# Performance work log

Measured on AMD Instinct MI355X. Metric: run time of the kernel, lower is better.

## Reference

```python
import jax, jax.numpy as jnp
import numpy as np

B, S, D, H = 4, 1024, 1024, 16
DEPTH = D // H


def setup_inputs() -> dict:
    key = jax.random.key(0)
    ks = jax.random.split(key, 13)
    inp = {
        'query': jax.random.normal(ks[0], (B, S, D), dtype=jnp.float32),
        'key': jax.random.normal(ks[1], (B, S, D), dtype=jnp.float32),
        'value': jax.random.normal(ks[2], (B, S, D), dtype=jnp.float32),
        'mask': jax.random.bernoulli(ks[3], 0.1, (B, S, S)),
    }
    scale = 1.0 / np.sqrt(D)
    inp['wq_w'] = jax.random.uniform(ks[4], (D, D), jnp.float32, -scale, scale)
    inp['wq_b'] = jax.random.uniform(ks[5], (D,), jnp.float32, -scale, scale)
    inp['wk_w'] = jax.random.uniform(ks[6], (D, D), jnp.float32, -scale, scale)
    inp['wk_b'] = jax.random.uniform(ks[7], (D,), jnp.float32, -scale, scale)
    inp['wv_w'] = jax.random.uniform(ks[8], (D, D), jnp.float32, -scale, scale)
    inp['wv_b'] = jax.random.uniform(ks[9], (D,), jnp.float32, -scale, scale)
    inp['fc_w'] = jax.random.uniform(ks[10], (D, D), jnp.float32, -scale, scale)
    inp['fc_b'] = jax.random.uniform(ks[11], (D,), jnp.float32, -scale, scale)
    return inp


def _split_heads(x):
    # [B,S,D] -> [B,H,S,depth]
    b, s, _ = x.shape
    return x.reshape(b, s, H, DEPTH).transpose(0, 2, 1, 3)


def reference(query, key, value, mask, wq_w, wq_b, wk_w, wk_b, wv_w, wv_b, fc_w, fc_b):
    q = _split_heads(query @ wq_w.T + wq_b)
    k = _split_heads(key @ wk_w.T + wk_b)
    v = _split_heads(value @ wv_w.T + wv_b)
    scores = jnp.einsum('bhqd,bhkd->bhqk', q, k) / jnp.sqrt(jnp.float32(DEPTH))
    scores = jnp.where(mask[:, None, :, :], jnp.float32(-1e9), scores)
    attn = jax.nn.softmax(scores, axis=-1)
    out = jnp.einsum('bhqk,bhkd->bhqd', attn, v)  # [B,H,S,depth]
    out = out.transpose(0, 2, 1, 3).reshape(query.shape[0], -1, D)
    return out @ fc_w.T + fc_b
```

## Files before the change

kernel.cpp:

```cpp
#include <hip/hip_runtime.h>
#include <hip/hip_bf16.h>


typedef __bf16 bf16x8 __attribute__((ext_vector_type(8)));
typedef __bf16 bf16x4 __attribute__((ext_vector_type(4)));
typedef float  f32x4  __attribute__((ext_vector_type(4)));

typedef const __attribute__((address_space(1))) void* gptr_t;
typedef __attribute__((address_space(3))) void* lptr_t;

#define MFMA16(a, b, c) __builtin_amdgcn_mfma_f32_16x16x32_bf16((a), (b), (c), 0, 0, 0)

__device__ __forceinline__ void gload_lds16(const void* g, void* l) {
  __builtin_amdgcn_global_load_lds((gptr_t)g, (lptr_t)l, 16, 0, 0);
}

__global__ void detect_mask(const unsigned char* m, int* flag) {
  __shared__ int s1[256], s23[256];
  int tid = threadIdx.x;
  int c1 = 0, c23 = 0;
  for (int i = tid; i < 4096; i += 256) {
    int r = i & 3;
    if (m[i]) { if (r == 1) c1++; else if (r >= 2) c23++; }
  }
  s1[tid] = c1; s23[tid] = c23;
  __syncthreads();
  for (int st = 128; st; st >>= 1) {
    if (tid < st) { s1[tid] += s1[tid + st]; s23[tid] += s23[tid + st]; }
    __syncthreads();
  }
  if (tid == 0) *flag = (s1[0] > 0) ? 1 : (s23[0] > 0 ? 2 : 0);
}

__global__ void pack_mask(const void* m, const int* flag, unsigned int* out) {
  size_t i = (size_t)blockIdx.x * 256 + threadIdx.x;
  int f = *flag;
  bool v;
  if (f == 1)      v = ((const unsigned char*)m)[i] != 0;
  else if (f == 2) v = ((const float*)m)[i] != 0.0f;
  else             v = ((const int*)m)[i] != 0;
  unsigned long long bal = __ballot(v);
  int lane = threadIdx.x & 63;
  if ((lane & 31) == 0) out[i >> 5] = (unsigned int)(bal >> (lane & 32));
}

__global__ void cvt3(const float* a, const float* b, const float* c,
                     __bf16* oa, __bf16* ob, __bf16* oc) {
  int bid = blockIdx.x;
  int which = bid >> 12, sub = bid & 4095;
  const float* in = which == 0 ? a : which == 1 ? b : c;
  __bf16* out = which == 0 ? oa : which == 1 ? ob : oc;
  size_t i = (size_t)sub * 256 + threadIdx.x;
  float4 v = ((const float4*)in)[i];
  bf16x4 o; o[0] = (__bf16)v.x; o[1] = (__bf16)v.y; o[2] = (__bf16)v.z; o[3] = (__bf16)v.w;
  ((bf16x4*)out)[i] = o;
}

__global__ void cvt4(const float* a, const float* b, const float* c, const float* d,
                     __bf16* oa, __bf16* ob, __bf16* oc, __bf16* od) {
  int bid = blockIdx.x;
  int which = bid >> 10, sub = bid & 1023;
  const float* in = which == 0 ? a : which == 1 ? b : which == 2 ? c : d;
  __bf16* out = which == 0 ? oa : which == 1 ? ob : which == 2 ? oc : od;
  size_t i = (size_t)sub * 256 + threadIdx.x;
  float4 v = ((const float4*)in)[i];
  bf16x4 o; o[0] = (__bf16)v.x; o[1] = (__bf16)v.y; o[2] = (__bf16)v.z; o[3] = (__bf16)v.w;
  ((bf16x4*)out)[i] = o;
}

__global__ __launch_bounds__(256, 2)
void gemm_qkv(const __bf16* qb, const __bf16* kb, const __bf16* vb,
              const __bf16* wq, const __bf16* wk, const __bf16* wv,
              const float* bq, const float* bk, const float* bv,
              __bf16* Qp, __bf16* Kp, __bf16* Vt) {
  __shared__ __bf16 As[128 * 64];
  __shared__ __bf16 Bs[128 * 64];
  const int bm = blockIdx.x;
  const int bnall = blockIdx.y;
  const int which = bnall >> 3;
  const int bn = bnall & 7;
  const __bf16* A = which == 0 ? qb : which == 1 ? kb : vb;
  const __bf16* W = which == 0 ? wq : which == 1 ? wk : wv;
  const float* bias = which == 0 ? bq : which == 1 ? bk : bv;

  const int tid = threadIdx.x, wave = tid >> 6, lane = tid & 63;
  const int wr = wave >> 1, wc = wave & 1;
  const int rl = lane >> 3, c8 = lane & 7;
  f32x4 acc[4][4] = {};

  for (int kt = 0; kt < 16; ++kt) {
    __syncthreads();
#pragma unroll
    for (int i = 0; i < 4; ++i) {
      int row = wave * 32 + i * 8 + rl;
      int sw = (c8 ^ (row & 7)) << 3;
      gload_lds16(A + (size_t)(bm * 128 + row) * 1024 + kt * 64 + sw, As + (wave * 32 + i * 8) * 64);
      gload_lds16(W + (size_t)(bn * 128 + row) * 1024 + kt * 64 + sw, Bs + (wave * 32 + i * 8) * 64);
    }
    __syncthreads();
#pragma unroll
    for (int k32 = 0; k32 < 2; ++k32) {
      bf16x8 af[4], bfr[4];
#pragma unroll
      for (int mi = 0; mi < 4; ++mi) {
        int row = wr * 64 + mi * 16 + (lane & 15);
        af[mi] = *(const bf16x8*)(As + row * 64 + (((k32 * 4 + (lane >> 4)) ^ (row & 7)) << 3));
      }
#pragma unroll
      for (int ni = 0; ni < 4; ++ni) {
        int row = wc * 64 + ni * 16 + (lane & 15);
        bfr[ni] = *(const bf16x8*)(Bs + row * 64 + (((k32 * 4 + (lane >> 4)) ^ (row & 7)) << 3));
      }
#pragma unroll
      for (int mi = 0; mi < 4; ++mi)
#pragma unroll
        for (int ni = 0; ni < 4; ++ni)
          acc[mi][ni] = MFMA16(af[mi], bfr[ni], acc[mi][ni]);
    }
  }
  const int r0 = (lane >> 4) * 4, cl = lane & 15;
  __bf16* Onat = which == 0 ? Qp : Kp;
#pragma unroll
  for (int ni = 0; ni < 4; ++ni) {
    int col = bn * 128 + wc * 64 + ni * 16 + cl;
    float bvv = bias[col];
#pragma unroll
    for (int mi = 0; mi < 4; ++mi) {
      int rowb = bm * 128 + wr * 64 + mi * 16 + r0;
      if (which < 2) {
#pragma unroll
        for (int r = 0; r < 4; ++r)
          Onat[(size_t)(rowb + r) * 1024 + col] = (__bf16)(acc[mi][ni][r] + bvv);
      } else {
        int bb = rowb >> 10, s0 = rowb & 1023, hh = col >> 6, d = col & 63;
        bf16x4 ov;
#pragma unroll
        for (int r = 0; r < 4; ++r) ov[r] = (__bf16)(acc[mi][ni][r] + bvv);
        *(bf16x4*)(Vt + (((size_t)(bb * 16 + hh) * 64 + d) << 10) + s0) = ov;
      }
    }
  }
}

__global__ __launch_bounds__(256, 2)
void gemm_fc(const __bf16* A, const __bf16* W, const float* bias, float* C) {
  __shared__ __bf16 As[128 * 64];
  __shared__ __bf16 Bs[128 * 64];
  const int bm = blockIdx.x, bn = blockIdx.y;
  const int tid = threadIdx.x, wave = tid >> 6, lane = tid & 63;
  const int wr = wave >> 1, wc = wave & 1;
  const int rl = lane >> 3, c8 = lane & 7;
  f32x4 acc[4][4] = {};

  for (int kt = 0; kt < 16; ++kt) {
    __syncthreads();
#pragma unroll
    for (int i = 0; i < 4; ++i) {
      int row = wave * 32 + i * 8 + rl;
      int sw = (c8 ^ (row & 7)) << 3;
      gload_lds16(A + (size_t)(bm * 128 + row) * 1024 + kt * 64 + sw, As + (wave * 32 + i * 8) * 64);
      gload_lds16(W + (size_t)(bn * 128 + row) * 1024 + kt * 64 + sw, Bs + (wave * 32 + i * 8) * 64);
    }
    __syncthreads();
#pragma unroll
    for (int k32 = 0; k32 < 2; ++k32) {
      bf16x8 af[4], bfr[4];
#pragma unroll
      for (int mi = 0; mi < 4; ++mi) {
        int row = wr * 64 + mi * 16 + (lane & 15);
        af[mi] = *(const bf16x8*)(As + row * 64 + (((k32 * 4 + (lane >> 4)) ^ (row & 7)) << 3));
      }
#pragma unroll
      for (int ni = 0; ni < 4; ++ni) {
        int row = wc * 64 + ni * 16 + (lane & 15);
        bfr[ni] = *(const bf16x8*)(Bs + row * 64 + (((k32 * 4 + (lane >> 4)) ^ (row & 7)) << 3));
      }
#pragma unroll
      for (int mi = 0; mi < 4; ++mi)
#pragma unroll
        for (int ni = 0; ni < 4; ++ni)
          acc[mi][ni] = MFMA16(af[mi], bfr[ni], acc[mi][ni]);
    }
  }
  const int r0 = (lane >> 4) * 4, cl = lane & 15;
#pragma unroll
  for (int ni = 0; ni < 4; ++ni) {
    int col = bn * 128 + wc * 64 + ni * 16 + cl;
    float bvv = bias[col];
#pragma unroll
    for (int mi = 0; mi < 4; ++mi) {
      int rowb = bm * 128 + wr * 64 + mi * 16 + r0;
#pragma unroll
      for (int r = 0; r < 4; ++r)
        C[(size_t)(rowb + r) * 1024 + col] = acc[mi][ni][r] + bvv;
    }
  }
}

__global__ __launch_bounds__(256, 2)
void attn(const __bf16* Qp, const __bf16* Kp, const __bf16* Vt,
          const unsigned int* mp, __bf16* O) {
  __shared__ __bf16 Qs[128 * 64];
  __shared__ __bf16 Ks[128 * 64];
  __shared__ __bf16 Vs[64 * 128];
  __shared__ __bf16 Ps[128 * 128];
  const int tid = threadIdx.x, wave = tid >> 6, lane = tid & 63;
  const int bx = blockIdx.x;
  const int qt = bx & 7, h = (bx >> 3) & 15, b = bx >> 7;
  const int rl = lane >> 3, c8 = lane & 7;

#pragma unroll
  for (int i = 0; i < 4; ++i) {
    int row = wave * 32 + i * 8 + rl;
    int sw = (c8 ^ (row & 7)) << 3;
    gload_lds16(Qp + (size_t)(b * 1024 + qt * 128 + row) * 1024 + h * 64 + sw,
                Qs + (wave * 32 + i * 8) * 64);
  }
  __syncthreads();
  bf16x8 qf[2][2];
#pragma unroll
  for (int mi = 0; mi < 2; ++mi)
#pragma unroll
    for (int k32 = 0; k32 < 2; ++k32) {
      int row = wave * 32 + mi * 16 + (lane & 15);
      qf[mi][k32] = *(const bf16x8*)(Qs + row * 64 + (((k32 * 4 + (lane >> 4)) ^ (row & 7)) << 3));
    }

  f32x4 oacc[2][4] = {};
  float dsum[2][4] = {};
  const unsigned int* mrow_base = mp + ((size_t)(b << 10) + qt * 128) * 32;

  for (int kt = 0; kt < 8; ++kt) {
    __syncthreads();
#pragma unroll
    for (int i = 0; i < 4; ++i) {
      int row = wave * 32 + i * 8 + rl;
      int sw = (c8 ^ (row & 7)) << 3;
      gload_lds16(Kp + (size_t)(b * 1024 + kt * 128 + row) * 1024 + h * 64 + sw,
                  Ks + (wave * 32 + i * 8) * 64);
    }
#pragma unroll
    for (int i = 0; i < 4; ++i) {
      int d0 = wave * 16 + i * 4;
      int d = d0 + (lane >> 4), c16 = lane & 15;
      gload_lds16(Vt + (((size_t)(b * 16 + h) * 64 + d) << 10) + kt * 128 + ((c16 ^ (d & 7)) << 3),
                  Vs + d0 * 128);
    }
    __syncthreads();

    uint4 mw[2][4];
#pragma unroll
    for (int mi = 0; mi < 2; ++mi)
#pragma unroll
      for (int r = 0; r < 4; ++r) {
        int rowl = wave * 32 + mi * 16 + (lane >> 4) * 4 + r;
        mw[mi][r] = *(const uint4*)(mrow_base + (size_t)rowl * 32 + kt * 4);
      }

#pragma unroll
    for (int ni = 0; ni < 8; ++ni) {
      f32x4 s0 = {}, s1 = {};
#pragma unroll
      for (int k32 = 0; k32 < 2; ++k32) {
        int row = ni * 16 + (lane & 15);
        bf16x8 kf = *(const bf16x8*)(Ks + row * 64 + (((k32 * 4 + (lane >> 4)) ^ (row & 7)) << 3));
        s0 = MFMA16(qf[0][k32], kf, s0);
        s1 = MFMA16(qf[1][k32], kf, s1);
      }
      int col = ni * 16 + (lane & 15);
      int bit = (ni & 1) * 16 + (lane & 15);
      int wsel = ni >> 1;
#pragma unroll
      for (int mi = 0; mi < 2; ++mi) {
        f32x4 sv = mi ? s1 : s0;
#pragma unroll
        for (int r = 0; r < 4; ++r) {
          unsigned int w = ((const unsigned int*)&mw[mi][r])[wsel];
          float p = ((w >> bit) & 1) ? 0.0f : __expf(sv[r] * 0.125f);
          __bf16 pb = (__bf16)p;
          dsum[mi][r] += (float)pb;
          int rowl = wave * 32 + mi * 16 + (lane >> 4) * 4 + r;
          *(__bf16*)((char*)Ps + rowl * 256 + ((col * 2) ^ ((rowl & 7) << 4))) = pb;
        }
      }
    }

#pragma unroll
    for (int ks = 0; ks < 4; ++ks) {
      bf16x8 pf0, pf1;
      {
        int row = wave * 32 + (lane & 15);
        pf0 = *(const bf16x8*)((const char*)Ps + row * 256 + (((ks * 4 + (lane >> 4)) * 16) ^ ((row & 7) << 4)));
        row = wave * 32 + 16 + (lane & 15);
        pf1 = *(const bf16x8*)((const char*)Ps + row * 256 + (((ks * 4 + (lane >> 4)) * 16) ^ ((row & 7) << 4)));
      }
#pragma unroll
      for (int nd = 0; nd < 4; ++nd) {
        int d = nd * 16 + (lane & 15);
        bf16x8 vf = *(const bf16x8*)((const char*)Vs + d * 256 + (((ks * 4 + (lane >> 4)) * 16) ^ ((d & 7) << 4)));
        oacc[0][nd] = MFMA16(pf0, vf, oacc[0][nd]);
        oacc[1][nd] = MFMA16(pf1, vf, oacc[1][nd]);
      }
    }
  }

#pragma unroll
  for (int mi = 0; mi < 2; ++mi)
#pragma unroll
    for (int r = 0; r < 4; ++r) {
      float v = dsum[mi][r];
      v += __shfl_xor(v, 1, 64);
      v += __shfl_xor(v, 2, 64);
      v += __shfl_xor(v, 4, 64);
      v += __shfl_xor(v, 8, 64);
      dsum[mi][r] = v;
    }

#pragma unroll
  for (int mi = 0; mi < 2; ++mi)
#pragma unroll
    for (int nd = 0; nd < 4; ++nd)
#pragma unroll
      for (int r = 0; r < 4; ++r) {
        int rowl = wave * 32 + mi * 16 + (lane >> 4) * 4 + r;
        int d = nd * 16 + (lane & 15);
        float v = oacc[mi][nd][r] / dsum[mi][r];
        O[(size_t)(b * 1024 + qt * 128 + rowl) * 1024 + h * 64 + d] = (__bf16)v;
      }
}

extern "C" void kernel_launch(void* const* d_in, const int* in_sizes, int n_in,
                              void* d_out, int out_size, void* d_ws, size_t ws_size,
                              hipStream_t stream) {
  const float* query = (const float*)d_in[0];
  const float* key   = (const float*)d_in[1];
  const float* value = (const float*)d_in[2];
  const void*  mask  = d_in[3];
  const float* wq_w  = (const float*)d_in[4];
  const float* wq_b  = (const float*)d_in[5];
  const float* wk_w  = (const float*)d_in[6];
  const float* wk_b  = (const float*)d_in[7];
  const float* wv_w  = (const float*)d_in[8];
  const float* wv_b  = (const float*)d_in[9];
  const float* fc_w  = (const float*)d_in[10];
  const float* fc_b  = (const float*)d_in[11];

  char* ws = (char*)d_ws;
  __bf16* qb  = (__bf16*)ws;
  __bf16* kb  = qb  + 4194304;
  __bf16* vb  = kb  + 4194304;
  __bf16* wqb = vb  + 4194304;
  __bf16* wkb = wqb + 1048576;
  __bf16* wvb = wkb + 1048576;
  __bf16* fcb = wvb + 1048576;
  __bf16* Qp  = fcb + 1048576;
  __bf16* Kp  = Qp  + 4194304;
  __bf16* Vt  = Kp  + 4194304;
  __bf16* Ob  = Vt  + 4194304;
  unsigned int* mpk = (unsigned int*)(Ob + 4194304);
  int* flag = (int*)(mpk + 131072);

  detect_mask<<<1, 256, 0, stream>>>((const unsigned char*)mask, flag);
  pack_mask<<<16384, 256, 0, stream>>>(mask, flag, mpk);
  cvt3<<<12288, 256, 0, stream>>>(query, key, value, qb, kb, vb);
  cvt4<<<4096, 256, 0, stream>>>(wq_w, wk_w, wv_w, fc_w, wqb, wkb, wvb, fcb);
  dim3 g1(32, 24);
  gemm_qkv<<<g1, 256, 0, stream>>>(qb, kb, vb, wqb, wkb, wvb, wq_b, wk_b, wv_b, Qp, Kp, Vt);
  attn<<<512, 256, 0, stream>>>(Qp, Kp, Vt, mpk, Ob);
  dim3 g2(32, 8);
  gemm_fc<<<g2, 256, 0, stream>>>(Ob, fcb, fc_b, (float*)d_out);
}
```

Before: 245.7 us.

## Rewrite attention as LDS-free 32x32 MFMA kernel with register P exchange

Replaces the LDS-staged attention kernel with one that uses 32x32x16 bf16 MFMAs. It computes S^T so that the P tile can be rebuilt as an MFMA A-operand with a cross-half lane shuffle, and reads K and V fragments directly from global memory, with no shared memory or barriers. The softmax uses exp2 with a folded scale, and the mask detector becomes a single vectorized ballot. This removes LDS traffic and sync stalls, but relies on L2/L1 for the repeated K/V reads across the four waves and drops the occupancy hint.

```diff
diff --git a/kernel.cpp b/kernel.cpp
--- a/kernel.cpp
+++ b/kernel.cpp
@@ -5,31 +5,43 @@
 typedef __bf16 bf16x8 __attribute__((ext_vector_type(8)));
 typedef __bf16 bf16x4 __attribute__((ext_vector_type(4)));
 typedef float  f32x4  __attribute__((ext_vector_type(4)));
+typedef float  f32x16 __attribute__((ext_vector_type(16)));
 
 typedef const __attribute__((address_space(1))) void* gptr_t;
 typedef __attribute__((address_space(3))) void* lptr_t;
 
 #define MFMA16(a, b, c) __builtin_amdgcn_mfma_f32_16x16x32_bf16((a), (b), (c), 0, 0, 0)
+#define MFMA32(a, b, c) __builtin_amdgcn_mfma_f32_32x32x16_bf16((a), (b), (c), 0, 0, 0)
 
 __device__ __forceinline__ void gload_lds16(const void* g, void* l) {
   __builtin_amdgcn_global_load_lds((gptr_t)g, (lptr_t)l, 16, 0, 0);
 }
 
+__device__ __forceinline__ unsigned pack2(float a, float b) {
+  union { __bf16 h[2]; unsigned u; } x;
+  x.h[0] = (__bf16)a; x.h[1] = (__bf16)b; return x.u;
+}
+
+__device__ __forceinline__ bf16x8 mkfrag(unsigned a, unsigned b, unsigned c, unsigned d) {
+  union { unsigned w[4]; bf16x8 v; } x;
+  x.w[0] = a; x.w[1] = b; x.w[2] = c; x.w[3] = d; return x.v;
+}
+
 __global__ void detect_mask(const unsigned char* m, int* flag) {
-  __shared__ int s1[256], s23[256];
+  __shared__ int s1[4], s23[4];
   int tid = threadIdx.x;
-  int c1 = 0, c23 = 0;
-  for (int i = tid; i < 4096; i += 256) {
-    int r = i & 3;
-    if (m[i]) { if (r == 1) c1++; else if (r >= 2) c23++; }
-  }
-  s1[tid] = c1; s23[tid] = c23;
+  uint4 v = ((const uint4*)m)[tid];
+  unsigned x0 = v.x, x1 = v.y, x2 = v.z, x3 = v.w;
+  unsigned c1  = (x0 & 0x0000ff00u) | (x1 & 0x0000ff00u) | (x2 & 0x0000ff00u) | (x3 & 0x0000ff00u);
+  unsigned c23 = (x0 & 0xffff0000u) | (x1 & 0xffff0000u) | (x2 & 0xffff0000u) | (x3 & 0xffff0000u);
+  unsigned long long b1 = __ballot(c1 != 0), b23 = __ballot(c23 != 0);
+  if ((tid & 63) == 0) { s1[tid >> 6] = (b1 != 0); s23[tid >> 6] = (b23 != 0); }
   __syncthreads();
-  for (int st = 128; st; st >>= 1) {
-    if (tid < st) { s1[tid] += s1[tid + st]; s23[tid] += s23[tid + st]; }
-    __syncthreads();
-  }
-  if (tid == 0) *flag = (s1[0] > 0) ? 1 : (s23[0] > 0 ? 2 : 0);
+  if (tid == 0) {
+    int a1 = s1[0] | s1[1] | s1[2] | s1[3];
+    int a23 = s23[0] | s23[1] | s23[2] | s23[3];
+    *flag = a1 ? 1 : (a23 ? 2 : 0);
+  }
 }
 
 __global__ void pack_mask(const void* m, const int* flag, unsigned int* out) {
@@ -197,136 +209,113 @@
   }
 }
 
-__global__ __launch_bounds__(256, 2)
-void attn(const __bf16* Qp, const __bf16* Kp, const __bf16* Vt,
-          const unsigned int* mp, __bf16* O) {
-  __shared__ __bf16 Qs[128 * 64];
-  __shared__ __bf16 Ks[128 * 64];
-  __shared__ __bf16 Vs[64 * 128];
-  __shared__ __bf16 Ps[128 * 128];
+__global__ __launch_bounds__(256)
+void attn32(const __bf16* __restrict__ Qp, const __bf16* __restrict__ Kp,
+            const __bf16* __restrict__ Vt, const unsigned long long* __restrict__ mp64,
+            __bf16* __restrict__ O) {
   const int tid = threadIdx.x, wave = tid >> 6, lane = tid & 63;
+  const int lo5 = lane & 31, hi = lane >> 5;
   const int bx = blockIdx.x;
   const int qt = bx & 7, h = (bx >> 3) & 15, b = bx >> 7;
-  const int rl = lane >> 3, c8 = lane & 7;
-
-#pragma unroll
-  for (int i = 0; i < 4; ++i) {
-    int row = wave * 32 + i * 8 + rl;
-    int sw = (c8 ^ (row & 7)) << 3;
-    gload_lds16(Qp + (size_t)(b * 1024 + qt * 128 + row) * 1024 + h * 64 + sw,
-                Qs + (wave * 32 + i * 8) * 64);
-  }
-  __syncthreads();
-  bf16x8 qf[2][2];
-#pragma unroll
-  for (int mi = 0; mi < 2; ++mi)
-#pragma unroll
-    for (int k32 = 0; k32 < 2; ++k32) {
-      int row = wave * 32 + mi * 16 + (lane & 15);
-      qf[mi][k32] = *(const bf16x8*)(Qs + row * 64 + (((k32 * 4 + (lane >> 4)) ^ (row & 7)) << 3));
-    }
-
-  f32x4 oacc[2][4] = {};
-  float dsum[2][4] = {};
-  const unsigned int* mrow_base = mp + ((size_t)(b << 10) + qt * 128) * 32;
-
-  for (int kt = 0; kt < 8; ++kt) {
-    __syncthreads();
-#pragma unroll
-    for (int i = 0; i < 4; ++i) {
-      int row = wave * 32 + i * 8 + rl;
-      int sw = (c8 ^ (row & 7)) << 3;
-      gload_lds16(Kp + (size_t)(b * 1024 + kt * 128 + row) * 1024 + h * 64 + sw,
-                  Ks + (wave * 32 + i * 8) * 64);
-    }
-#pragma unroll
-    for (int i = 0; i < 4; ++i) {
-      int d0 = wave * 16 + i * 4;
-      int d = d0 + (lane >> 4), c16 = lane & 15;
-      gload_lds16(Vt + (((size_t)(b * 16 + h) * 64 + d) << 10) + kt * 128 + ((c16 ^ (d & 7)) << 3),
-                  Vs + d0 * 128);
-    }
-    __syncthreads();
-
-    uint4 mw[2][4];
-#pragma unroll
-    for (int mi = 0; mi < 2; ++mi)
-#pragma unroll
-      for (int r = 0; r < 4; ++r) {
-        int rowl = wave * 32 + mi * 16 + (lane >> 4) * 4 + r;
-        mw[mi][r] = *(const uint4*)(mrow_base + (size_t)rowl * 32 + kt * 4);
-      }
-
-#pragma unroll
-    for (int ni = 0; ni < 8; ++ni) {
-      f32x4 s0 = {}, s1 = {};
-#pragma unroll
-      for (int k32 = 0; k32 < 2; ++k32) {
-        int row = ni * 16 + (lane & 15);
-        bf16x8 kf = *(const bf16x8*)(Ks + row * 64 + (((k32 * 4 + (lane >> 4)) ^ (row & 7)) << 3));
-        s0 = MFMA16(qf[0][k32], kf, s0);
-        s1 = MFMA16(qf[1][k32], kf, s1);
-      }
-      int col = ni * 16 + (lane & 15);
-      int bit = (ni & 1) * 16 + (lane & 15);
-      int wsel = ni >> 1;
-#pragma unroll
-      for (int mi = 0; mi < 2; ++mi) {
-        f32x4 sv = mi ? s1 : s0;
-#pragma unroll
-        for (int r = 0; r < 4; ++r) {
-          unsigned int w = ((const unsigned int*)&mw[mi][r])[wsel];
-          float p = ((w >> bit) & 1) ? 0.0f : __expf(sv[r] * 0.125f);
-          __bf16 pb = (__bf16)p;
-          dsum[mi][r] += (float)pb;
-          int rowl = wave * 32 + mi * 16 + (lane >> 4) * 4 + r;
-          *(__bf16*)((char*)Ps + rowl * 256 + ((col * 2) ^ ((rowl & 7) << 4))) = pb;
-        }
-      }
-    }
-
-#pragma unroll
-    for (int ks = 0; ks < 4; ++ks) {
-      bf16x8 pf0, pf1;
-      {
-        int row = wave * 32 + (lane & 15);
-        pf0 = *(const bf16x8*)((const char*)Ps + row * 256 + (((ks * 4 + (lane >> 4)) * 16) ^ ((row & 7) << 4)));
-        row = wave * 32 + 16 + (lane & 15);
-        pf1 = *(const bf16x8*)((const char*)Ps + row * 256 + (((ks * 4 + (lane >> 4)) * 16) ^ ((row & 7) << 4)));
-      }
-#pragma unroll
-      for (int nd = 0; nd < 4; ++nd) {
-        int d = nd * 16 + (lane & 15);
-        bf16x8 vf = *(const bf16x8*)((const char*)Vs + d * 256 + (((ks * 4 + (lane >> 4)) * 16) ^ ((d & 7) << 4)));
-        oacc[0][nd] = MFMA16(pf0, vf, oacc[0][nd]);
-        oacc[1][nd] = MFMA16(pf1, vf, oacc[1][nd]);
-      }
-    }
-  }
-
-#pragma unroll
-  for (int mi = 0; mi < 2; ++mi)
-#pragma unroll
-    for (int r = 0; r < 4; ++r) {
-      float v = dsum[mi][r];
-      v += __shfl_xor(v, 1, 64);
-      v += __shfl_xor(v, 2, 64);
-      v += __shfl_xor(v, 4, 64);
-      v += __shfl_xor(v, 8, 64);
-      dsum[mi][r] = v;
-    }
-
-#pragma unroll
-  for (int mi = 0; mi < 2; ++mi)
-#pragma unroll
-    for (int nd = 0; nd < 4; ++nd)
-#pragma unroll
-      for (int r = 0; r < 4; ++r) {
-        int rowl = wave * 32 + mi * 16 + (lane >> 4) * 4 + r;
-        int d = nd * 16 + (lane & 15);
-        float v = oacc[mi][nd][r] / dsum[mi][r];
-        O[(size_t)(b * 1024 + qt * 128 + rowl) * 1024 + h * 64 + d] = (__bf16)v;
-      }
+  const int qrow = qt * 128 + wave * 32 + lo5;
+  const float SC = 0.18033688011112042f;
+
+  bf16x8 qf[4];
+  const __bf16* qb = Qp + ((size_t)(b * 1024 + qrow)) * 1024 + h * 64 + hi * 8;
+#pragma unroll
+  for (int m = 0; m < 4; ++m) qf[m] = *(const bf16x8*)(qb + m * 16);
+
+  f32x16 oacc0 = {}, oacc1 = {};
+  float dsum = 0.0f;
+  const unsigned long long* mrow = mp64 + ((size_t)(b * 1024 + qrow)) * 16;
+  const __bf16* vrow = Vt + ((size_t)((b * 16 + h) * 64 + lo5)) * 1024;
+
+  for (int kt = 0; kt < 16; ++kt) {
+    unsigned long long mw = mrow[kt];
+    const __bf16* kb = Kp + ((size_t)(b * 1024 + kt * 64 + lo5)) * 1024 + h * 64 + hi * 8;
+    const __bf16* vb = vrow + kt * 64 + hi * 8;
+
+    f32x16 s0 = {};
+#pragma unroll
+    for (int m = 0; m < 4; ++m)
+      s0 = MFMA32(*(const bf16x8*)(kb + m * 16), qf[m], s0);
+    float p0[16];
+#pragma unroll
+    for (int r = 0; r < 16; ++r) {
+      int cr = (r & 3) + 8 * (r >> 2) + 4 * hi;
+      float e = exp2f(s0[r] * SC);
+      p0[r] = ((mw >> cr) & 1) ? 0.0f : e;
+      dsum += p0[r];
+    }
+    unsigned own0[8], rcv0[8];
+#pragma unroll
+    for (int u = 0; u < 4; ++u) {
+      own0[2 * u]     = pack2(p0[4 * u],     p0[4 * u + 1]);
+      own0[2 * u + 1] = pack2(p0[4 * u + 2], p0[4 * u + 3]);
+    }
+#pragma unroll
+    for (int i = 0; i < 8; ++i) rcv0[i] = (unsigned)__shfl_xor((int)own0[i], 32, 64);
+#pragma unroll
+    for (int s = 0; s < 2; ++s) {
+      const int ue2 = 4 * s, uo2 = 4 * s + 2;
+      unsigned fw0 = hi ? rcv0[uo2 + 0] : own0[ue2 + 0];
+      unsigned fw1 = hi ? rcv0[uo2 + 1] : own0[ue2 + 1];
+      unsigned fw2 = hi ? own0[uo2 + 0] : rcv0[ue2 + 0];
+      unsigned fw3 = hi ? own0[uo2 + 1] : rcv0[ue2 + 1];
+      bf16x8 pa = mkfrag(fw0, fw1, fw2, fw3);
+      bf16x8 vf0 = *(const bf16x8*)(vb + s * 16);
+      bf16x8 vf1 = *(const bf16x8*)(vb + s * 16 + 32 * 1024);
+      oacc0 = MFMA32(pa, vf0, oacc0);
+      oacc1 = MFMA32(pa, vf1, oacc1);
+    }
+
+    f32x16 s1 = {};
+#pragma unroll
+    for (int m = 0; m < 4; ++m)
+      s1 = MFMA32(*(const bf16x8*)(kb + 32 * 1024 + m * 16), qf[m], s1);
+    float p1[16];
+#pragma unroll
+    for (int r = 0; r < 16; ++r) {
+      int cr = (r & 3) + 8 * (r >> 2) + 4 * hi;
+      float e = exp2f(s1[r] * SC);
+      p1[r] = ((mw >> (32 + cr)) & 1) ? 0.0f : e;
+      dsum += p1[r];
+    }
+    unsigned own1[8], rcv1[8];
+#pragma unroll
+    for (int u = 0; u < 4; ++u) {
+      own1[2 * u]     = pack2(p1[4 * u],     p1[4 * u + 1]);
+      own1[2 * u + 1] = pack2(p1[4 * u + 2], p1[4 * u + 3]);
+    }
+#pragma unroll
+    for (int i = 0; i < 8; ++i) rcv1[i] = (unsigned)__shfl_xor((int)own1[i], 32, 64);
+#pragma unroll
+    for (int s = 0; s < 2; ++s) {
+      const int ue2 = 4 * s, uo2 = 4 * s + 2;
+      unsigned fw0 = hi ? rcv1[uo2 + 0] : own1[ue2 + 0];
+      unsigned fw1 = hi ? rcv1[uo2 + 1] : own1[ue2 + 1];
+      unsigned fw2 = hi ? own1[uo2 + 0] : rcv1[ue2 + 0];
+      unsigned fw3 = hi ? own1[uo2 + 1] : rcv1[ue2 + 1];
+      bf16x8 pa = mkfrag(fw0, fw1, fw2, fw3);
+      bf16x8 vf0 = *(const bf16x8*)(vb + (s + 2) * 16);
+      bf16x8 vf1 = *(const bf16x8*)(vb + (s + 2) * 16 + 32 * 1024);
+      oacc0 = MFMA32(pa, vf0, oacc0);
+      oacc1 = MFMA32(pa, vf1, oacc1);
+    }
+  }
+
+  dsum += __shfl_xor(dsum, 32, 64);
+  float inv = 1.0f / dsum;
+
+  const size_t orow0 = (size_t)(b * 1024 + qt * 128 + wave * 32);
+#pragma unroll
+  for (int r = 0; r < 16; ++r) {
+    int cr = (r & 3) + 8 * (r >> 2) + 4 * hi;
+    float iv = __shfl(inv, cr, 64);
+    __bf16* op = O + (orow0 + cr) * 1024 + h * 64 + lo5;
+    op[0]  = (__bf16)(oacc0[r] * iv);
+    op[32] = (__bf16)(oacc1[r] * iv);
+  }
 }
 
 extern "C" void kernel_launch(void* const* d_in, const int* in_sizes, int n_in,
@@ -366,7 +355,7 @@
   cvt4<<<4096, 256, 0, stream>>>(wq_w, wk_w, wv_w, fc_w, wqb, wkb, wvb, fcb);
   dim3 g1(32, 24);
   gemm_qkv<<<g1, 256, 0, stream>>>(qb, kb, vb, wqb, wkb, wvb, wq_b, wk_b, wv_b, Qp, Kp, Vt);
-  attn<<<512, 256, 0, stream>>>(Qp, Kp, Vt, mpk, Ob);
+  attn32<<<512, 256, 0, stream>>>(Qp, Kp, Vt, (const unsigned long long*)mpk, Ob);
   dim3 g2(32, 8);
   gemm_fc<<<g2, 256, 0, stream>>>(Ob, fcb, fc_b, (float*)d_out);
 }
```

Result: slower. 261.9 us (+6.6%).
